# Kernel tuning notes

Measured on AMD Instinct MI355X. Metric: run time of the kernel, lower is better.

Reference implementation:

```python
import jax, jax.numpy as jnp
import numpy as np

HIDDEN = 2048
N_HEADS = 16
N_KV_HEADS = 8
HEAD_DIM = 128
MROPE_SECTION = [8, 8, 24, 24]          # sums to HEAD_DIM // 2
ROPE_THETA = 10000.0
B, S, CTX = 4, 1024, 2048
# per-frequency section index (which of the 4 position streams drives each freq)
_SEC_IDX = np.repeat(np.arange(len(MROPE_SECTION)), MROPE_SECTION)  # (HEAD_DIM//2,)


def setup_inputs() -> dict:
    key = jax.random.key(0)
    ks = jax.random.split(key, 6)
    return {
        "hidden_states": jax.random.normal(ks[0], (B, S, HIDDEN), jnp.float32),
        "Wqkv": jax.random.normal(ks[1], (HIDDEN, (N_HEADS + 2 * N_KV_HEADS) * HEAD_DIM), jnp.float32) * 0.02,
        "Wo": jax.random.normal(ks[2], (N_HEADS * HEAD_DIM, HIDDEN), jnp.float32) * 0.02,
        "ctx_k": jax.random.normal(ks[3], (B, CTX, N_KV_HEADS, HEAD_DIM), jnp.float32),
        "ctx_v": jax.random.normal(ks[4], (B, CTX, N_KV_HEADS, HEAD_DIM), jnp.float32),
        "position_ids": jax.random.randint(ks[5], (len(MROPE_SECTION), S), 0, CTX + S, jnp.int32),
    }


def _mrope_cos_sin(position_ids):
    # position_ids: (n_sections, S) int -> cos/sin of shape (S, HEAD_DIM)
    half = HEAD_DIM // 2
    inv_freq = 1.0 / (ROPE_THETA ** (jnp.arange(0, half, dtype=jnp.float32) * 2.0 / HEAD_DIM))
    freqs = position_ids.astype(jnp.float32)[:, :, None] * inv_freq[None, None, :]  # (4, S, half)
    sec = jnp.asarray(_SEC_IDX)[None, None, :]                                       # (1, 1, half)
    f = jnp.take_along_axis(freqs, jnp.broadcast_to(sec, (1,) + freqs.shape[1:]), axis=0)[0]  # (S, half)
    emb = jnp.concatenate([f, f], axis=-1)  # (S, HEAD_DIM)
    return jnp.cos(emb), jnp.sin(emb)


def _rotate_half(x):
    h = x.shape[-1] // 2
    return jnp.concatenate([-x[..., h:], x[..., :h]], axis=-1)


def reference(hidden_states, Wqkv, Wo, ctx_k, ctx_v, position_ids):
    b, s, _ = hidden_states.shape
    q_size = N_HEADS * HEAD_DIM
    kv_size = N_KV_HEADS * HEAD_DIM
    qkv = hidden_states @ Wqkv  # (B, S, q+2kv)
    q = qkv[..., :q_size].reshape(b, s, N_HEADS, HEAD_DIM)
    k = qkv[..., q_size:q_size + kv_size].reshape(b, s, N_KV_HEADS, HEAD_DIM)
    v = qkv[..., q_size + kv_size:].reshape(b, s, N_KV_HEADS, HEAD_DIM)

    cos, sin = _mrope_cos_sin(position_ids)        # (S, D) each
    cos = cos[None, :, None, :]
    sin = sin[None, :, None, :]
    q = q * cos + _rotate_half(q) * sin
    k = k * cos + _rotate_half(k) * sin

    # KV-cache concat along sequence dim
    k = jnp.concatenate([ctx_k, k], axis=1)        # (B, CTX+S, KV, D)
    v = jnp.concatenate([ctx_v, v], axis=1)

    # GQA: expand kv heads to query heads
    rep = N_HEADS // N_KV_HEADS
    k = jnp.repeat(k, rep, axis=2)                 # (B, T, H, D)
    v = jnp.repeat(v, rep, axis=2)

    scale = HEAD_DIM ** -0.5
    scores = jnp.einsum("bqhd,bkhd->bhqk", q, k) * scale  # non-causal
    probs = jax.nn.softmax(scores, axis=-1)
    out = jnp.einsum("bhqk,bkhd->bqhd", probs, v)  # (B, S, H, D)
    out = out.reshape(b, s, N_HEADS * HEAD_DIM)
    return out @ Wo
```

## Files before the change

kernel.cpp:

```cpp
#include <hip/hip_runtime.h>
#include <hip/hip_bf16.h>
#include <stdint.h>

#define NH 16
#define NKV 8
#define HD 128
#define BB 4
#define SS 1024
#define CTXL 2048
#define LT 3072
#define HID 2048
#define QKVN 4096
#define MROWS 4096

typedef __hip_bfloat16 bf16;
using f32x4 = __attribute__((ext_vector_type(4))) float;
using s16x8 = __attribute__((ext_vector_type(8))) short;

#define MFMA(a, b, c) __builtin_amdgcn_mfma_f32_16x16x32_bf16((a), (b), (c), 0, 0, 0)

__device__ __forceinline__ void gload_lds16(const void* g, void* l) {
  __builtin_amdgcn_global_load_lds((const __attribute__((address_space(1))) void*)g,
                                   (__attribute__((address_space(3))) void*)l, 16, 0, 0);
}

__device__ __forceinline__ void store_bf8(bf16* dst, const float* f) {
  bf16 tmp[8];
#pragma unroll
  for (int j = 0; j < 8; ++j) tmp[j] = __float2bfloat16(f[j]);
  __builtin_memcpy((void*)dst, (const void*)tmp, 16);
}

__device__ __forceinline__ float bf2f(short x) {
  unsigned int u = ((unsigned int)(unsigned short)x) << 16;
  float f;
  __builtin_memcpy(&f, &u, 4);
  return f;
}

#define P1_CVT 4096
#define P1_WQ (P1_CVT + 8192)
#define P1_WO (P1_WQ + 4096)
#define P1_RT (P1_WO + 256)
#define P1_CK (P1_RT + 4096)
#define P1_CV (P1_CK + 8192)

__global__ void prep1(const float* __restrict__ hs, const float* __restrict__ Wqkv,
                      const float* __restrict__ Wo, const float* __restrict__ ck,
                      const float* __restrict__ cv, const int* __restrict__ pid,
                      bf16* __restrict__ Hb, bf16* __restrict__ WqT,
                      bf16* __restrict__ WoT, bf16* __restrict__ Kf,
                      bf16* __restrict__ Vt, float* __restrict__ cosT,
                      float* __restrict__ sinT) {
  __shared__ float tile[32][33];
  const int blk = blockIdx.x, thr = threadIdx.x;
  if (blk < P1_CVT) {
    size_t tid = (size_t)blk * 256 + thr;
    const float4* p = (const float4*)(hs + tid * 8);
    float4 a = p[0], b = p[1];
    float f[8] = {a.x, a.y, a.z, a.w, b.x, b.y, b.z, b.w};
    store_bf8(Hb + tid * 8, f);
  } else if (blk < P1_WQ) {
    int j = blk - P1_CVT;
    int c0 = (j & 127) * 32, r0 = (j >> 7) * 32;
    int tx = thr & 31, ty = thr >> 5;
#pragma unroll
    for (int i = 0; i < 32; i += 8)
      tile[ty + i][tx] = Wqkv[(size_t)(r0 + ty + i) * QKVN + c0 + tx];
    __syncthreads();
#pragma unroll
    for (int i = 0; i < 32; i += 8)
      WqT[(size_t)(c0 + ty + i) * HID + r0 + tx] = __float2bfloat16(tile[tx][ty + i]);
  } else if (blk < P1_WO) {
    int j = blk - P1_WQ;
    int c0 = (j & 63) * 32, r0 = (j >> 6) * 32;
    int tx = thr & 31, ty = thr >> 5;
#pragma unroll
    for (int i = 0; i < 32; i += 8)
      tile[ty + i][tx] = Wo[(size_t)(r0 + ty + i) * 2048 + c0 + tx];
    __syncthreads();
#pragma unroll
    for (int i = 0; i < 32; i += 8)
      WoT[(size_t)(c0 + ty + i) * 2048 + r0 + tx] = __float2bfloat16(tile[tx][ty + i]);
  } else if (blk < P1_RT) {
    int tid = (blk - P1_WO) * 256 + thr;
    int j = tid & 63, s = tid >> 6;
    int sec = (j < 8) ? 0 : (j < 16) ? 1 : (j < 40) ? 2 : 3;
    float pos = (float)pid[sec * SS + s];
    float inv = __expf(-(float)j * 0.14391156831212787f);
    float a = pos * inv;
    cosT[tid] = cosf(a);
    sinT[tid] = sinf(a);
  } else if (blk < P1_CK) {
    int tid = (blk - P1_RT) * 256 + thr;
    int d8 = tid & 15, l = (tid >> 4) & 2047, h = (tid >> 15) & 7, b = tid >> 18;
    const float* s = ck + (((size_t)b * CTXL + l) * NKV + h) * HD + d8 * 8;
    const float4* p = (const float4*)s;
    float4 a = p[0], bb = p[1];
    float f[8] = {a.x, a.y, a.z, a.w, bb.x, bb.y, bb.z, bb.w};
    store_bf8(Kf + (((size_t)(b * NKV + h)) * LT + l) * HD + d8 * 8, f);
  } else {
    int j = blk - P1_CK;
    int l0 = (j & 63) * 32, d0 = ((j >> 6) & 3) * 32;
    int bz = j >> 8, b = bz >> 3, h = bz & 7;
    int tx = thr & 31, ty = thr >> 5;
#pragma unroll
    for (int i = 0; i < 32; i += 8)
      tile[ty + i][tx] =
          cv[(((size_t)b * CTXL + l0 + ty + i) * NKV + h) * HD + d0 + tx];
    __syncthreads();
#pragma unroll
    for (int i = 0; i < 32; i += 8)
      Vt[(((size_t)(b * NKV + h)) * HD + d0 + ty + i) * LT + l0 + tx] =
          __float2bfloat16(tile[tx][ty + i]);
  }
}


__global__ __launch_bounds__(512, 1) void gemm_qkv(
    const bf16* __restrict__ A, const bf16* __restrict__ BT,
    bf16* __restrict__ qkv, bf16* __restrict__ Kf, bf16* __restrict__ Vt,
    const float* __restrict__ cosT, const float* __restrict__ sinT) {
  __shared__ __attribute__((aligned(16))) char smem[132096];
  bf16* lds = (bf16*)smem;
#define lAp(s, hf) (lds + ((s)*2 + (hf)) * 8192)
#define lBp(s, hf) (lds + 32768 + ((s)*2 + (hf)) * 8192)
  const int K = HID;
  const int t = threadIdx.x;
  const int lane = t & 63, w = t >> 6;
  const int wr = w >> 2, wc = w & 3;
  const int lrow = lane & 15, kgrp = lane >> 4;
  const int lin = blockIdx.y * gridDim.x + blockIdx.x;
  const int qq = (gridDim.x * gridDim.y) >> 3;
  const int swz = (lin & 7) * qq + (lin >> 3);
  const int bx = swz % gridDim.x, by = swz / gridDim.x;
  const int m0 = by * 256, n0 = bx * 256;
  const f32x4 fz = {0.f, 0.f, 0.f, 0.f};
  f32x4 acc[8][4];
#pragma unroll
  for (int i = 0; i < 8; ++i)
#pragma unroll
    for (int j = 0; j < 4; ++j) acc[i][j] = fz;

#define STAGEH(sslot, skt, isB, shalf)                                        \
  do {                                                                        \
    _Pragma("unroll") for (int c = 0; c < 2; ++c) {                           \
      int row = w * 16 + c * 8 + (lane >> 3);                                 \
      int sch = (lane & 7) ^ (lane >> 3);                                     \
      const bf16* src =                                                       \
          (isB) ? (BT + (size_t)(n0 + (shalf)*128 + row) * K + (skt)*64 + sch * 8) \
                : (A + (size_t)(m0 + (shalf)*128 + row) * K + (skt)*64 + sch * 8); \
      bf16* dst = ((isB) ? lBp((sslot), (shalf)) : lAp((sslot), (shalf))) +   \
                  (w * 16 + c * 8) * 64;                                      \
      gload_lds16(src, dst);                                                  \
    }                                                                         \
  } while (0)

#define PHASE(cslot, qm, qn, DOST, sslot, skt, isB, shalf)                    \
  do {                                                                        \
    if (DOST) {                                                               \
      STAGEH(sslot, skt, isB, shalf);                                         \
      asm volatile("s_waitcnt vmcnt(2)" ::: "memory");                        \
    } else {                                                                  \
      asm volatile("s_waitcnt vmcnt(0)" ::: "memory");                        \
    }                                                                         \
    __builtin_amdgcn_s_barrier();                                             \
    __builtin_amdgcn_sched_barrier(0);                                        \
    s16x8 af_[4][2], bf_[2][2];                                               \
    _Pragma("unroll") for (int fi = 0; fi < 4; ++fi)                          \
        _Pragma("unroll") for (int ks = 0; ks < 2; ++ks) {                    \
      int row = (qm)*64 + fi * 16 + lrow;                                     \
      af_[fi][ks] = *(const s16x8*)&lAp(cslot, wr)[row * 64 +                 \
                                                   ((ks * 4 + kgrp) ^ (lrow & 7)) * 8]; \
    }                                                                         \
    _Pragma("unroll") for (int fj = 0; fj < 2; ++fj)                          \
        _Pragma("unroll") for (int ks = 0; ks < 2; ++ks) {                    \
      int col = (wc & 1) * 64 + (qn)*32 + fj * 16 + lrow;                     \
      bf_[fj][ks] = *(const s16x8*)&lBp(cslot, wc >> 1)[col * 64 +            \
                                                        ((ks * 4 + kgrp) ^ (lrow & 7)) * 8]; \
    }                                                                         \
    asm volatile("s_waitcnt lgkmcnt(0)" ::: "memory");                        \
    __builtin_amdgcn_sched_barrier(0);                                        \
    __builtin_amdgcn_s_setprio(1);                                            \
    _Pragma("unroll") for (int fi = 0; fi < 4; ++fi)                          \
        _Pragma("unroll") for (int fj = 0; fj < 2; ++fj)                      \
            _Pragma("unroll") for (int ks = 0; ks < 2; ++ks)                  \
                acc[(qm)*4 + fi][(qn)*2 + fj] =                               \
        MFMA(af_[fi][ks], bf_[fj][ks], acc[(qm)*4 + fi][(qn)*2 + fj]);        \
    __builtin_amdgcn_s_setprio(0);                                            \
    __builtin_amdgcn_s_barrier();                                             \
  } while (0)

  STAGEH(0, 0, 0, 0);
  STAGEH(0, 0, 1, 0);
  STAGEH(0, 0, 0, 1);
  STAGEH(0, 0, 1, 1);
  asm volatile("s_waitcnt vmcnt(0)" ::: "memory");
  __builtin_amdgcn_s_barrier();

  for (int kt = 0; kt < 32; kt += 2) {
    PHASE(0, 0, 0, true, 1, kt + 1, 0, 0);
    PHASE(0, 1, 0, true, 1, kt + 1, 1, 0);
    PHASE(0, 0, 1, true, 1, kt + 1, 0, 1);
    PHASE(0, 1, 1, true, 1, kt + 1, 1, 1);
    const bool d2 = (kt + 2 < 32);
    PHASE(1, 0, 0, d2, 0, kt + 2, 0, 0);
    PHASE(1, 1, 0, d2, 0, kt + 2, 1, 0);
    PHASE(1, 0, 1, d2, 0, kt + 2, 0, 1);
    PHASE(1, 1, 1, d2, 0, kt + 2, 1, 1);
  }
#undef PHASE
#undef STAGEH

  const int b = m0 >> 10, s0 = m0 & 1023;
  if (n0 < 2048) {
#pragma unroll
    for (int fm = 0; fm < 8; ++fm)
#pragma unroll
      for (int fn = 0; fn < 4; ++fn)
#pragma unroll
        for (int r = 0; r < 4; ++r) {
          int row = m0 + wr * 128 + fm * 16 + kgrp * 4 + r;
          int col = n0 + wc * 64 + fn * 16 + lrow;
          qkv[(size_t)row * QKVN + col] = __float2bfloat16(acc[fm][fn][r]);
        }
  } else {
    float* stage = (float*)smem;
#pragma unroll 1
    for (int hh = 0; hh < 2; ++hh) {
      __syncthreads();
      if ((wc >> 1) == hh) {
#pragma unroll
        for (int fm = 0; fm < 8; ++fm)
#pragma unroll
          for (int fn = 0; fn < 4; ++fn)
#pragma unroll
            for (int r = 0; r < 4; ++r) {
              int rr = wr * 128 + fm * 16 + kgrp * 4 + r;
              int cc = (wc & 1) * 64 + fn * 16 + lrow;
              stage[rr * 129 + cc] = acc[fm][fn][r];
            }
      }
      __syncthreads();
      if (n0 < 3072) {
        int h = ((n0 - 2048) >> 7) + hh;
#pragma unroll 4
        for (int it = 0; it < 32; ++it) {
          int idx = it * 512 + t;
          int r = idx >> 6, j = idx & 63;
          float x1 = stage[r * 129 + j], x2 = stage[r * 129 + j + 64];
          int s = s0 + r;
          float c = cosT[s * 64 + j], sn = sinT[s * 64 + j];
          bf16* dst = Kf + ((size_t)(b * NKV + h) * LT + CTXL + s) * HD;
          dst[j] = __float2bfloat16(x1 * c - x2 * sn);
          dst[j + 64] = __float2bfloat16(x2 * c + x1 * sn);
        }
      } else {
        int h = ((n0 - 3072) >> 7) + hh;
#pragma unroll 4
        for (int it = 0; it < 64; ++it) {
          int idx = it * 512 + t;
          int soff = idx & 255, d = idx >> 8;
          Vt[((size_t)(b * NKV + h) * HD + d) * LT + CTXL + s0 + soff] =
              __float2bfloat16(stage[soff * 129 + d]);
        }
      }
    }
  }
#undef lAp
#undef lBp
}

template <typename OT>
__global__ __launch_bounds__(512, 1) void gemm_bt(const bf16* __restrict__ A,
                                                  const bf16* __restrict__ BT,
                                                  OT* __restrict__ C, int M, int N,
                                                  int K) {
  __shared__ __attribute__((aligned(16))) bf16 lA[3][256][64];
  __shared__ __attribute__((aligned(16))) bf16 lB[3][128][64];
  const int t = threadIdx.x;
  const int lane = t & 63, w = t >> 6;
  const int wr = w >> 1, wc = w & 1;
  const int lrow = lane & 15, kgrp = lane >> 4;
  const int rchk = lrow & 7;
  const int lin = blockIdx.y * gridDim.x + blockIdx.x;
  const int qq = (gridDim.x * gridDim.y) >> 3;
  const int swz = (lin & 7) * qq + (lin >> 3);
  const int bx = swz % gridDim.x, by = swz / gridDim.x;
  const int m0 = by * 256, n0 = bx * 128;
  const int srow = lane >> 3;
  const int schk = (lane & 7) ^ srow;
  const f32x4 fz = {0.f, 0.f, 0.f, 0.f};
  f32x4 acc[4][4];
#pragma unroll
  for (int i = 0; i < 4; ++i)
#pragma unroll
    for (int j = 0; j < 4; ++j) acc[i][j] = fz;
  const int NTK = K >> 6;

#define GSTAGE(ib, kt)                                                      \
  do {                                                                      \
    _Pragma("unroll") for (int c = 0; c < 4; ++c) {                         \
      int ra = c * 64 + w * 8 + srow;                                       \
      gload_lds16(A + (size_t)(m0 + ra) * K + (kt)*64 + schk * 8,           \
                  &lA[ib][c * 64 + w * 8][0]);                              \
    }                                                                       \
    _Pragma("unroll") for (int c = 0; c < 2; ++c) {                         \
      int rb = c * 64 + w * 8 + srow;                                       \
      gload_lds16(BT + (size_t)(n0 + rb) * K + (kt)*64 + schk * 8,          \
                  &lB[ib][c * 64 + w * 8][0]);                              \
    }                                                                       \
  } while (0)

  GSTAGE(0, 0);
  GSTAGE(1, 1);
  int ib = 0;
  for (int kt = 0; kt < NTK; ++kt) {
    if (kt + 1 < NTK)
      asm volatile("s_waitcnt vmcnt(6) lgkmcnt(0)" ::: "memory");
    else
      asm volatile("s_waitcnt vmcnt(0) lgkmcnt(0)" ::: "memory");
    __builtin_amdgcn_s_barrier();
    __builtin_amdgcn_sched_barrier(0);
    if (kt + 2 < NTK) {
      int ib2 = ib + 2;
      if (ib2 >= 3) ib2 -= 3;
      GSTAGE(ib2, kt + 2);
    }
#pragma unroll
    for (int kk = 0; kk < 2; ++kk) {
      s16x8 af[4], bf[4];
#pragma unroll
      for (int i = 0; i < 4; ++i)
        af[i] = *(const s16x8*)&lA[ib][wr * 64 + i * 16 + lrow]
                                     [(((kk << 2) + kgrp) ^ rchk) * 8];
#pragma unroll
      for (int j = 0; j < 4; ++j)
        bf[j] = *(const s16x8*)&lB[ib][wc * 64 + j * 16 + lrow]
                                     [(((kk << 2) + kgrp) ^ rchk) * 8];
      __builtin_amdgcn_s_setprio(1);
#pragma unroll
      for (int i = 0; i < 4; ++i)
#pragma unroll
        for (int j = 0; j < 4; ++j) acc[i][j] = MFMA(af[i], bf[j], acc[i][j]);
      __builtin_amdgcn_s_setprio(0);
    }
    ++ib;
    if (ib >= 3) ib = 0;
  }
#undef GSTAGE

#pragma unroll
  for (int i = 0; i < 4; ++i)
#pragma unroll
    for (int j = 0; j < 4; ++j)
#pragma unroll
      for (int r = 0; r < 4; ++r) {
        int row = m0 + wr * 64 + i * 16 + kgrp * 4 + r;
        int col = n0 + wc * 64 + j * 16 + lrow;
        float v = acc[i][j][r];
        if constexpr (sizeof(OT) == 2)
          C[(size_t)row * N + col] = __float2bfloat16(v);
        else
          C[(size_t)row * N + col] = v;
      }
}

#define PSTR 72
#define KVB 128
#define NTT 24
#define SCALE2 0.1275174335919605f

__global__ __launch_bounds__(512, 2) void flash_attn(
    const bf16* __restrict__ qkv, const float* __restrict__ cosT,
    const float* __restrict__ sinT, const bf16* __restrict__ Kf,
    const bf16* __restrict__ Vt, bf16* __restrict__ O) {
  __shared__ __attribute__((aligned(16))) bf16 Kl[2][128][128];
  __shared__ __attribute__((aligned(16))) bf16 Vl[2][128][128];
  __shared__ __attribute__((aligned(16))) bf16 P_lds[8][16][PSTR];
  const int t = threadIdx.x, lane = t & 63, w = t >> 6;
  const int id = blockIdx.x;
  const int b = id >> 6, hk = id & 7;
  const int h = (hk << 1) | ((id >> 5) & 1);
  const int qb = (id >> 3) & 3;
  const int lrow = lane & 15, kgrp = lane >> 4;
  const bf16* Kp = Kf + (size_t)(b * NKV + hk) * LT * HD;
  const bf16* Vp = Vt + (size_t)(b * NKV + hk) * HD * LT;

  s16x8 qf[2][4];
#pragma unroll
  for (int f = 0; f < 2; ++f) {
    int srw_i = qb * 256 + w * 32 + f * 16 + lrow;
    const bf16* qrow = qkv + ((size_t)b * SS + srw_i) * QKVN + h * HD;
    s16x8 qr[4];
#pragma unroll
    for (int kd = 0; kd < 4; ++kd)
      qr[kd] = *(const s16x8*)&qrow[kd * 32 + kgrp * 8];
    const float* crow = cosT + srw_i * 64 + kgrp * 8;
    const float* srow = sinT + srw_i * 64 + kgrp * 8;
    float qv[4][8], cc[2][8], ssv[2][8];
#pragma unroll
    for (int kd = 0; kd < 4; ++kd)
#pragma unroll
      for (int j = 0; j < 8; ++j) qv[kd][j] = bf2f(qr[kd][j]);
#pragma unroll
    for (int g = 0; g < 2; ++g)
#pragma unroll
      for (int j = 0; j < 8; ++j) {
        cc[g][j] = crow[g * 32 + j];
        ssv[g][j] = srow[g * 32 + j];
      }
    bf16 o[4][8];
#pragma unroll
    for (int j = 0; j < 8; ++j) {
      o[0][j] = __float2bfloat16(qv[0][j] * cc[0][j] - qv[2][j] * ssv[0][j]);
      o[1][j] = __float2bfloat16(qv[1][j] * cc[1][j] - qv[3][j] * ssv[1][j]);
      o[2][j] = __float2bfloat16(qv[2][j] * cc[0][j] + qv[0][j] * ssv[0][j]);
      o[3][j] = __float2bfloat16(qv[3][j] * cc[1][j] + qv[1][j] * ssv[1][j]);
    }
#pragma unroll
    for (int kd = 0; kd < 4; ++kd) __builtin_memcpy(&qf[f][kd], o[kd], 16);
  }

  const f32x4 fz = {0.f, 0.f, 0.f, 0.f};
  f32x4 acc[2][8];
#pragma unroll
  for (int f = 0; f < 2; ++f)
#pragma unroll
    for (int i = 0; i < 8; ++i) acc[f][i] = fz;
  float m_[2] = {-1e30f, -1e30f}, l_[2] = {0.f, 0.f};

#define STAGE_K(buf, l0)                                                        \
  do {                                                                          \
    _Pragma("unroll") for (int c = 0; c < 4; ++c) {                             \
      int row = w * 16 + c * 4 + (lane >> 4);                                   \
      gload_lds16(Kp + (size_t)((l0) + row) * HD + ((lane & 15) ^ (row & 15)) * 8, \
                  &Kl[buf][w * 16 + c * 4][0]);                                 \
    }                                                                           \
  } while (0)
#define STAGE_V(buf, l0)                                                        \
  do {                                                                          \
    _Pragma("unroll") for (int c = 0; c < 4; ++c) {                             \
      int d = w * 16 + c * 4 + (lane >> 4);                                     \
      gload_lds16(Vp + (size_t)d * LT + (l0) + ((lane & 15) ^ (d & 15)) * 8,    \
                  &Vl[buf][w * 16 + c * 4][0]);                                 \
    }                                                                           \
  } while (0)

  STAGE_K(0, 0);
  STAGE_V(0, 0);
  __syncthreads();

  for (int tt = 0; tt < NTT; ++tt) {
    const int cur = tt & 1;
    if (tt + 1 < NTT) {
      STAGE_K(cur ^ 1, (tt + 1) * KVB);
      STAGE_V(cur ^ 1, (tt + 1) * KVB);
    }

    f32x4 sc[2][8];
#pragma unroll
    for (int f = 0; f < 2; ++f)
#pragma unroll
      for (int cf = 0; cf < 8; ++cf) sc[f][cf] = fz;
#pragma unroll
    for (int cf = 0; cf < 8; ++cf)
#pragma unroll
      for (int kd = 0; kd < 4; ++kd) {
        s16x8 kb =
            *(const s16x8*)&Kl[cur][cf * 16 + lrow][((kd * 4 + kgrp) ^ lrow) * 8];
#pragma unroll
        for (int f = 0; f < 2; ++f) sc[f][cf] = MFMA(kb, qf[f][kd], sc[f][cf]);
      }

    float mxv[2];
#pragma unroll
    for (int f = 0; f < 2; ++f) {
      float mx = sc[f][0][0];
#pragma unroll
      for (int cf = 0; cf < 8; ++cf)
#pragma unroll
        for (int r = 0; r < 4; ++r) mx = fmaxf(mx, sc[f][cf][r]);
      mx *= SCALE2;
      mx = fmaxf(mx, __shfl_xor(mx, 16, 64));
      mx = fmaxf(mx, __shfl_xor(mx, 32, 64));
      mxv[f] = mx;
    }
    bool nb = (mxv[0] > m_[0] + 8.f) || (mxv[1] > m_[1] + 8.f);
    if (__any(nb)) {
#pragma unroll
      for (int f = 0; f < 2; ++f) {
        float mn = fmaxf(m_[f], mxv[f]);
        float so = exp2f(m_[f] - mn);
        m_[f] = mn;
        l_[f] *= so;
        float sob[4];
#pragma unroll
        for (int r = 0; r < 4; ++r) sob[r] = __shfl(so, kgrp * 4 + r, 16);
#pragma unroll
        for (int nd = 0; nd < 8; ++nd)
#pragma unroll
          for (int r = 0; r < 4; ++r) acc[f][nd][r] *= sob[r];
      }
    }

    float lp[2] = {0.f, 0.f};
#pragma unroll
    for (int half = 0; half < 2; ++half) {
      s16x8 pa[2][2];
#pragma unroll
      for (int f = 0; f < 2; ++f) {
#pragma unroll
        for (int cf = 0; cf < 4; ++cf) {
          int cfs = half * 4 + cf;
          bf16 pk[4];
#pragma unroll
          for (int r = 0; r < 4; ++r) {
            float p = exp2f(sc[f][cfs][r] * SCALE2 - m_[f]);
            lp[f] += p;
            pk[r] = __float2bfloat16(p);
          }
          __builtin_memcpy((void*)&P_lds[w][lrow][cf * 16 + kgrp * 4], pk, 8);
        }
#pragma unroll
        for (int kc = 0; kc < 2; ++kc)
          pa[f][kc] = *(const s16x8*)&P_lds[w][lrow][kc * 32 + kgrp * 8];
      }
#pragma unroll
      for (int nd = 0; nd < 8; ++nd)
#pragma unroll
        for (int kc = 0; kc < 2; ++kc) {
          s16x8 vb = *(const s16x8*)&Vl[cur][nd * 16 + lrow]
                                       [((half * 8 + kc * 4 + kgrp) ^ lrow) * 8];
#pragma unroll
          for (int f = 0; f < 2; ++f) acc[f][nd] = MFMA(pa[f][kc], vb, acc[f][nd]);
        }
    }
#pragma unroll
    for (int f = 0; f < 2; ++f) l_[f] += lp[f];

    __syncthreads();
  }
#undef STAGE_K
#undef STAGE_V

  float li[2][4];
#pragma unroll
  for (int f = 0; f < 2; ++f) {
    float lv = l_[f];
    lv += __shfl_xor(lv, 16, 64);
    lv += __shfl_xor(lv, 32, 64);
#pragma unroll
    for (int r = 0; r < 4; ++r) li[f][r] = 1.f / __shfl(lv, kgrp * 4 + r, 16);
  }
#pragma unroll
  for (int f = 0; f < 2; ++f)
#pragma unroll
    for (int nd = 0; nd < 8; ++nd)
#pragma unroll
      for (int r = 0; r < 4; ++r) {
        int row = qb * 256 + w * 32 + f * 16 + kgrp * 4 + r;
        O[((size_t)b * SS + row) * 2048 + h * HD + nd * 16 + lrow] =
            __float2bfloat16(acc[f][nd][r] * li[f][r]);
      }
}


extern "C" void kernel_launch(void* const* d_in, const int* in_sizes, int n_in,
                              void* d_out, int out_size, void* d_ws, size_t ws_size,
                              hipStream_t stream) {
  const float* hs = (const float*)d_in[0];
  const float* Wqkv = (const float*)d_in[1];
  const float* Wo = (const float*)d_in[2];
  const float* ctx_k = (const float*)d_in[3];
  const float* ctx_v = (const float*)d_in[4];
  const int* pid = (const int*)d_in[5];
  float* out = (float*)d_out;
  char* ws = (char*)d_ws;

  bf16* Hb = (bf16*)(ws);
  bf16* WqT = (bf16*)(ws + 16777216);
  bf16* WoT = (bf16*)(ws + 33554432);
  bf16* qkv = (bf16*)(ws + 41943040);
  bf16* Kfull = (bf16*)(ws + 92274688);
  bf16* Vt = (bf16*)(ws + 117440512);
  float* cosT = (float*)(ws + 142606336);
  float* sinT = (float*)(ws + 142606336 + 262144);
  bf16* attn = Hb;

  prep1<<<P1_CV, 256, 0, stream>>>(hs, Wqkv, Wo, ctx_k, ctx_v, pid, Hb, WqT, WoT,
                                   Kfull, Vt, cosT, sinT);
  gemm_qkv<<<dim3(QKVN / 256, MROWS / 256), 512, 0, stream>>>(
      Hb, WqT, qkv, Kfull, Vt, cosT, sinT);
  flash_attn<<<256, 512, 0, stream>>>(qkv, cosT, sinT, Kfull, Vt, attn);
  gemm_bt<float><<<dim3(2048 / 128, MROWS / 256), 512, 0, stream>>>(
      attn, WoT, out, MROWS, 2048, HID);
}
```

Measured before the change: 292.6 us.

## Move ctx K/V and Wo conversion into QKV GEMM launch as extra blocks

The ctx_k/ctx_v bf16 conversion and the Wo transpose are moved out of the prep kernel and appended as extra blocks to the QKV GEMM launch, so this memory-bound work can run alongside the compute-bound GEMM tiles. The prep kernel shrinks and uses 512-thread blocks, each doing two transpose tiles. The GEMM grid becomes 1D with a hardcoded swizzle. A risk is that the extra blocks request the GEMM's full 132KB LDS allocation and launch-bounds occupancy of 1, which limits how many can be resident per CU.

After: 313.4 us. +7.1%, slower.

```diff
diff --git a/kernel.cpp b/kernel.cpp
--- a/kernel.cpp
+++ b/kernel.cpp
@@ -38,52 +38,36 @@
   return f;
 }
 
-#define P1_CVT 4096
-#define P1_WQ (P1_CVT + 8192)
-#define P1_WO (P1_WQ + 4096)
-#define P1_RT (P1_WO + 256)
-#define P1_CK (P1_RT + 4096)
-#define P1_CV (P1_CK + 8192)
+#define P1_CVT 2048
+#define P1_WQ (P1_CVT + 4096)
+#define P1_RT (P1_WQ + 128)
 
 __global__ void prep1(const float* __restrict__ hs, const float* __restrict__ Wqkv,
-                      const float* __restrict__ Wo, const float* __restrict__ ck,
-                      const float* __restrict__ cv, const int* __restrict__ pid,
-                      bf16* __restrict__ Hb, bf16* __restrict__ WqT,
-                      bf16* __restrict__ WoT, bf16* __restrict__ Kf,
-                      bf16* __restrict__ Vt, float* __restrict__ cosT,
+                      const int* __restrict__ pid, bf16* __restrict__ Hb,
+                      bf16* __restrict__ WqT, float* __restrict__ cosT,
                       float* __restrict__ sinT) {
-  __shared__ float tile[32][33];
-  const int blk = blockIdx.x, thr = threadIdx.x;
+  __shared__ float tile[2][32][33];
+  const int blk = blockIdx.x, t = threadIdx.x;
   if (blk < P1_CVT) {
-    size_t tid = (size_t)blk * 256 + thr;
+    size_t tid = (size_t)blk * 512 + t;
     const float4* p = (const float4*)(hs + tid * 8);
     float4 a = p[0], b = p[1];
     float f[8] = {a.x, a.y, a.z, a.w, b.x, b.y, b.z, b.w};
     store_bf8(Hb + tid * 8, f);
   } else if (blk < P1_WQ) {
-    int j = blk - P1_CVT;
-    int c0 = (j & 127) * 32, r0 = (j >> 7) * 32;
-    int tx = thr & 31, ty = thr >> 5;
+    int j2 = (blk - P1_CVT) * 2 + (t >> 8);
+    int c0 = (j2 & 127) * 32, r0 = (j2 >> 7) * 32;
+    int tt = t & 255, tx = tt & 31, ty = tt >> 5, sl = t >> 8;
 #pragma unroll
     for (int i = 0; i < 32; i += 8)
-      tile[ty + i][tx] = Wqkv[(size_t)(r0 + ty + i) * QKVN + c0 + tx];
+      tile[sl][ty + i][tx] = Wqkv[(size_t)(r0 + ty + i) * QKVN + c0 + tx];
     __syncthreads();
 #pragma unroll
     for (int i = 0; i < 32; i += 8)
-      WqT[(size_t)(c0 + ty + i) * HID + r0 + tx] = __float2bfloat16(tile[tx][ty + i]);
-  } else if (blk < P1_WO) {
-    int j = blk - P1_WQ;
-    int c0 = (j & 63) * 32, r0 = (j >> 6) * 32;
-    int tx = thr & 31, ty = thr >> 5;
-#pragma unroll
-    for (int i = 0; i < 32; i += 8)
-      tile[ty + i][tx] = Wo[(size_t)(r0 + ty + i) * 2048 + c0 + tx];
-    __syncthreads();
-#pragma unroll
-    for (int i = 0; i < 32; i += 8)
-      WoT[(size_t)(c0 + ty + i) * 2048 + r0 + tx] = __float2bfloat16(tile[tx][ty + i]);
-  } else if (blk < P1_RT) {
-    int tid = (blk - P1_WO) * 256 + thr;
+      WqT[(size_t)(c0 + ty + i) * HID + r0 + tx] =
+          __float2bfloat16(tile[sl][tx][ty + i]);
+  } else {
+    int tid = (blk - P1_WQ) * 512 + t;
     int j = tid & 63, s = tid >> 6;
     int sec = (j < 8) ? 0 : (j < 16) ? 1 : (j < 40) ? 2 : 3;
     float pos = (float)pid[sec * SS + s];
@@ -91,49 +75,75 @@
     float a = pos * inv;
     cosT[tid] = cosf(a);
     sinT[tid] = sinf(a);
-  } else if (blk < P1_CK) {
-    int tid = (blk - P1_RT) * 256 + thr;
-    int d8 = tid & 15, l = (tid >> 4) & 2047, h = (tid >> 15) & 7, b = tid >> 18;
-    const float* s = ck + (((size_t)b * CTXL + l) * NKV + h) * HD + d8 * 8;
-    const float4* p = (const float4*)s;
-    float4 a = p[0], bb = p[1];
-    float f[8] = {a.x, a.y, a.z, a.w, bb.x, bb.y, bb.z, bb.w};
-    store_bf8(Kf + (((size_t)(b * NKV + h)) * LT + l) * HD + d8 * 8, f);
-  } else {
-    int j = blk - P1_CK;
-    int l0 = (j & 63) * 32, d0 = ((j >> 6) & 3) * 32;
-    int bz = j >> 8, b = bz >> 3, h = bz & 7;
-    int tx = thr & 31, ty = thr >> 5;
-#pragma unroll
-    for (int i = 0; i < 32; i += 8)
-      tile[ty + i][tx] =
-          cv[(((size_t)b * CTXL + l0 + ty + i) * NKV + h) * HD + d0 + tx];
-    __syncthreads();
-#pragma unroll
-    for (int i = 0; i < 32; i += 8)
-      Vt[(((size_t)(b * NKV + h)) * HD + d0 + ty + i) * LT + l0 + tx] =
-          __float2bfloat16(tile[tx][ty + i]);
-  }
-}
-
+  }
+}
+
+#define GQ_CK 256
+#define GQ_CV 2304
+#define GQ_WO 6400
+#define GQ_TOT 8448
 
 __global__ __launch_bounds__(512, 1) void gemm_qkv(
     const bf16* __restrict__ A, const bf16* __restrict__ BT,
     bf16* __restrict__ qkv, bf16* __restrict__ Kf, bf16* __restrict__ Vt,
-    const float* __restrict__ cosT, const float* __restrict__ sinT) {
+    const float* __restrict__ cosT, const float* __restrict__ sinT,
+    const float* __restrict__ Wo, bf16* __restrict__ WoT,
+    const float* __restrict__ ck, const float* __restrict__ cv) {
   __shared__ __attribute__((aligned(16))) char smem[132096];
+  const int id = blockIdx.x;
+  const int t = threadIdx.x;
+
+  if (id >= GQ_CK) {
+    if (id < GQ_CV) {
+      int tid = (id - GQ_CK) * 512 + t;
+      int d8 = tid & 15, l = (tid >> 4) & 2047, h = (tid >> 15) & 7, b = tid >> 18;
+      const float* s = ck + (((size_t)b * CTXL + l) * NKV + h) * HD + d8 * 8;
+      const float4* p = (const float4*)s;
+      float4 a = p[0], bb = p[1];
+      float f[8] = {a.x, a.y, a.z, a.w, bb.x, bb.y, bb.z, bb.w};
+      store_bf8(Kf + (((size_t)(b * NKV + h)) * LT + l) * HD + d8 * 8, f);
+    } else if (id < GQ_WO) {
+      float(*tile)[32][33] = (float(*)[32][33])smem;
+      int j2 = (id - GQ_CV) * 2 + (t >> 8);
+      int l0 = (j2 & 63) * 32, d0 = ((j2 >> 6) & 3) * 32;
+      int bz = j2 >> 8, b = bz >> 3, h = bz & 7;
+      int tt = t & 255, tx = tt & 31, ty = tt >> 5, sl = t >> 8;
+#pragma unroll
+      for (int i = 0; i < 32; i += 8)
+        tile[sl][ty + i][tx] =
+            cv[(((size_t)b * CTXL + l0 + ty + i) * NKV + h) * HD + d0 + tx];
+      __syncthreads();
+#pragma unroll
+      for (int i = 0; i < 32; i += 8)
+        Vt[(((size_t)(b * NKV + h)) * HD + d0 + ty + i) * LT + l0 + tx] =
+            __float2bfloat16(tile[sl][tx][ty + i]);
+    } else {
+      float(*tile)[32][33] = (float(*)[32][33])smem;
+      int j2 = (id - GQ_WO) * 2 + (t >> 8);
+      int c0 = (j2 & 63) * 32, r0 = (j2 >> 6) * 32;
+      int tt = t & 255, tx = tt & 31, ty = tt >> 5, sl = t >> 8;
+#pragma unroll
+      for (int i = 0; i < 32; i += 8)
+        tile[sl][ty + i][tx] = Wo[(size_t)(r0 + ty + i) * 2048 + c0 + tx];
+      __syncthreads();
+#pragma unroll
+      for (int i = 0; i < 32; i += 8)
+        WoT[(size_t)(c0 + ty + i) * 2048 + r0 + tx] =
+            __float2bfloat16(tile[sl][tx][ty + i]);
+    }
+    return;
+  }
+
   bf16* lds = (bf16*)smem;
 #define lAp(s, hf) (lds + ((s)*2 + (hf)) * 8192)
 #define lBp(s, hf) (lds + 32768 + ((s)*2 + (hf)) * 8192)
   const int K = HID;
-  const int t = threadIdx.x;
   const int lane = t & 63, w = t >> 6;
   const int wr = w >> 2, wc = w & 3;
   const int lrow = lane & 15, kgrp = lane >> 4;
-  const int lin = blockIdx.y * gridDim.x + blockIdx.x;
-  const int qq = (gridDim.x * gridDim.y) >> 3;
-  const int swz = (lin & 7) * qq + (lin >> 3);
-  const int bx = swz % gridDim.x, by = swz / gridDim.x;
+  const int lin = id;
+  const int swz = (lin & 7) * 32 + (lin >> 3);
+  const int bx = swz & 15, by = swz >> 4;
   const int m0 = by * 256, n0 = bx * 256;
   const f32x4 fz = {0.f, 0.f, 0.f, 0.f};
   f32x4 acc[8][4];
@@ -588,10 +598,9 @@
   float* sinT = (float*)(ws + 142606336 + 262144);
   bf16* attn = Hb;
 
-  prep1<<<P1_CV, 256, 0, stream>>>(hs, Wqkv, Wo, ctx_k, ctx_v, pid, Hb, WqT, WoT,
-                                   Kfull, Vt, cosT, sinT);
-  gemm_qkv<<<dim3(QKVN / 256, MROWS / 256), 512, 0, stream>>>(
-      Hb, WqT, qkv, Kfull, Vt, cosT, sinT);
+  prep1<<<P1_RT, 512, 0, stream>>>(hs, Wqkv, pid, Hb, WqT, cosT, sinT);
+  gemm_qkv<<<GQ_TOT, 512, 0, stream>>>(Hb, WqT, qkv, Kfull, Vt, cosT, sinT, Wo,
+                                       WoT, ctx_k, ctx_v);
   flash_attn<<<256, 512, 0, stream>>>(qkv, cosT, sinT, Kfull, Vt, attn);
   gemm_bt<float><<<dim3(2048 / 128, MROWS / 256), 512, 0, stream>>>(
       attn, WoT, out, MROWS, 2048, HID);
```

## Restructure output projection GEMM into phased double-buffered schedule with 2x4 warp grid

Applied to the files above, without the earlier changes.

Replaces the generic triple-buffered output-projection GEMM with a specialized kernel that uses two LDS buffers and splits each K-tile into four quarter phases. Global-to-LDS loads for the next tile are issued piecewise across those phases, each with its own vmcnt wait and barrier. The warp layout changes from 4x2 to 2x4, so each warp now computes 128x32 instead of 64x64. The aim is to interleave loads with MFMA work more finely and cut LDS footprint, at the cost of many more barriers per tile and a less square per-warp fragment shape.

After: 303.6 us. 3.8% more time.

```diff
diff --git a/kernel.cpp b/kernel.cpp
--- a/kernel.cpp
+++ b/kernel.cpp
@@ -116,7 +116,6 @@
   }
 }
 
-
 __global__ __launch_bounds__(512, 1) void gemm_qkv(
     const bf16* __restrict__ A, const bf16* __restrict__ BT,
     bf16* __restrict__ qkv, bf16* __restrict__ Kf, bf16* __restrict__ Vt,
@@ -271,98 +270,110 @@
 #undef lBp
 }
 
-template <typename OT>
-__global__ __launch_bounds__(512, 1) void gemm_bt(const bf16* __restrict__ A,
+__global__ __launch_bounds__(512, 1) void gemm_op(const bf16* __restrict__ A,
                                                   const bf16* __restrict__ BT,
-                                                  OT* __restrict__ C, int M, int N,
-                                                  int K) {
-  __shared__ __attribute__((aligned(16))) bf16 lA[3][256][64];
-  __shared__ __attribute__((aligned(16))) bf16 lB[3][128][64];
+                                                  float* __restrict__ C) {
+  __shared__ __attribute__((aligned(16))) bf16 lA[2][256][64];
+  __shared__ __attribute__((aligned(16))) bf16 lB[2][128][64];
+  const int K = HID, N = 2048;
   const int t = threadIdx.x;
   const int lane = t & 63, w = t >> 6;
-  const int wr = w >> 1, wc = w & 1;
+  const int wr = w >> 2, wc = w & 3;
   const int lrow = lane & 15, kgrp = lane >> 4;
-  const int rchk = lrow & 7;
   const int lin = blockIdx.y * gridDim.x + blockIdx.x;
   const int qq = (gridDim.x * gridDim.y) >> 3;
   const int swz = (lin & 7) * qq + (lin >> 3);
   const int bx = swz % gridDim.x, by = swz / gridDim.x;
   const int m0 = by * 256, n0 = bx * 128;
-  const int srow = lane >> 3;
-  const int schk = (lane & 7) ^ srow;
   const f32x4 fz = {0.f, 0.f, 0.f, 0.f};
-  f32x4 acc[4][4];
-#pragma unroll
-  for (int i = 0; i < 4; ++i)
-#pragma unroll
-    for (int j = 0; j < 4; ++j) acc[i][j] = fz;
-  const int NTK = K >> 6;
-
-#define GSTAGE(ib, kt)                                                      \
-  do {                                                                      \
-    _Pragma("unroll") for (int c = 0; c < 4; ++c) {                         \
-      int ra = c * 64 + w * 8 + srow;                                       \
-      gload_lds16(A + (size_t)(m0 + ra) * K + (kt)*64 + schk * 8,           \
-                  &lA[ib][c * 64 + w * 8][0]);                              \
-    }                                                                       \
-    _Pragma("unroll") for (int c = 0; c < 2; ++c) {                         \
-      int rb = c * 64 + w * 8 + srow;                                       \
-      gload_lds16(BT + (size_t)(n0 + rb) * K + (kt)*64 + schk * 8,          \
-                  &lB[ib][c * 64 + w * 8][0]);                              \
-    }                                                                       \
+  f32x4 acc[8][2];
+#pragma unroll
+  for (int i = 0; i < 8; ++i)
+#pragma unroll
+    for (int j = 0; j < 2; ++j) acc[i][j] = fz;
+
+#define OSA(sslot, skt, half)                                                 \
+  do {                                                                        \
+    _Pragma("unroll") for (int c = 0; c < 2; ++c) {                           \
+      int row = w * 16 + c * 8 + (lane >> 3);                                 \
+      int sch = (lane & 7) ^ (lane >> 3);                                     \
+      gload_lds16(A + (size_t)(m0 + (half)*128 + row) * K + (skt)*64 + sch * 8, \
+                  &lA[sslot][(half)*128 + w * 16 + c * 8][0]);                \
+    }                                                                         \
   } while (0)
-
-  GSTAGE(0, 0);
-  GSTAGE(1, 1);
-  int ib = 0;
-  for (int kt = 0; kt < NTK; ++kt) {
-    if (kt + 1 < NTK)
-      asm volatile("s_waitcnt vmcnt(6) lgkmcnt(0)" ::: "memory");
-    else
-      asm volatile("s_waitcnt vmcnt(0) lgkmcnt(0)" ::: "memory");
-    __builtin_amdgcn_s_barrier();
-    __builtin_amdgcn_sched_barrier(0);
-    if (kt + 2 < NTK) {
-      int ib2 = ib + 2;
-      if (ib2 >= 3) ib2 -= 3;
-      GSTAGE(ib2, kt + 2);
-    }
-#pragma unroll
-    for (int kk = 0; kk < 2; ++kk) {
-      s16x8 af[4], bf[4];
-#pragma unroll
-      for (int i = 0; i < 4; ++i)
-        af[i] = *(const s16x8*)&lA[ib][wr * 64 + i * 16 + lrow]
-                                     [(((kk << 2) + kgrp) ^ rchk) * 8];
-#pragma unroll
-      for (int j = 0; j < 4; ++j)
-        bf[j] = *(const s16x8*)&lB[ib][wc * 64 + j * 16 + lrow]
-                                     [(((kk << 2) + kgrp) ^ rchk) * 8];
-      __builtin_amdgcn_s_setprio(1);
-#pragma unroll
-      for (int i = 0; i < 4; ++i)
-#pragma unroll
-        for (int j = 0; j < 4; ++j) acc[i][j] = MFMA(af[i], bf[j], acc[i][j]);
-      __builtin_amdgcn_s_setprio(0);
-    }
-    ++ib;
-    if (ib >= 3) ib = 0;
+#define OSB(sslot, skt)                                                       \
+  do {                                                                        \
+    _Pragma("unroll") for (int c = 0; c < 2; ++c) {                           \
+      int row = w * 16 + c * 8 + (lane >> 3);                                 \
+      int sch = (lane & 7) ^ (lane >> 3);                                     \
+      gload_lds16(BT + (size_t)(n0 + row) * K + (skt)*64 + sch * 8,           \
+                  &lB[sslot][w * 16 + c * 8][0]);                             \
+    }                                                                         \
+  } while (0)
+
+#define OPHASE(cslot, qm, qn, DOST, STG, VMC)                                 \
+  do {                                                                        \
+    if (DOST) {                                                               \
+      STG;                                                                    \
+      asm volatile("s_waitcnt vmcnt(" #VMC ")" ::: "memory");                 \
+    } else {                                                                  \
+      asm volatile("s_waitcnt vmcnt(0)" ::: "memory");                        \
+    }                                                                         \
+    __builtin_amdgcn_s_barrier();                                             \
+    __builtin_amdgcn_sched_barrier(0);                                        \
+    s16x8 af_[4][2], bf_[2];                                                  \
+    _Pragma("unroll") for (int fi = 0; fi < 4; ++fi)                          \
+        _Pragma("unroll") for (int ks = 0; ks < 2; ++ks) {                    \
+      int row = wr * 128 + (qm)*64 + fi * 16 + lrow;                          \
+      af_[fi][ks] = *(const s16x8*)&lA[cslot][row]                            \
+                                       [((ks * 4 + kgrp) ^ (lrow & 7)) * 8];  \
+    }                                                                         \
+    _Pragma("unroll") for (int ks = 0; ks < 2; ++ks) {                        \
+      int col = wc * 32 + (qn)*16 + lrow;                                     \
+      bf_[ks] = *(const s16x8*)&lB[cslot][col]                                \
+                                   [((ks * 4 + kgrp) ^ (lrow & 7)) * 8];      \
+    }                                                                         \
+    asm volatile("s_waitcnt lgkmcnt(0)" ::: "memory");                        \
+    __builtin_amdgcn_sched_barrier(0);                                        \
+    __builtin_amdgcn_s_setprio(1);                                            \
+    _Pragma("unroll") for (int fi = 0; fi < 4; ++fi)                          \
+        _Pragma("unroll") for (int ks = 0; ks < 2; ++ks)                      \
+            acc[(qm)*4 + fi][qn] =                                            \
+        MFMA(af_[fi][ks], bf_[ks], acc[(qm)*4 + fi][qn]);                     \
+    __builtin_amdgcn_s_setprio(0);                                            \
+    __builtin_amdgcn_s_barrier();                                             \
+  } while (0)
+
+  OSA(0, 0, 0);
+  OSA(0, 0, 1);
+  OSB(0, 0);
+  asm volatile("s_waitcnt vmcnt(0)" ::: "memory");
+  __builtin_amdgcn_s_barrier();
+
+  for (int kt = 0; kt < 32; kt += 2) {
+    OPHASE(0, 0, 0, true, OSA(1, kt + 1, 0), 2);
+    OPHASE(0, 1, 0, true, OSA(1, kt + 1, 1), 4);
+    OPHASE(0, 0, 1, true, OSB(1, kt + 1), 6);
+    OPHASE(0, 1, 1, false, (void)0, 6);
+    const bool d2 = (kt + 2 < 32);
+    OPHASE(1, 0, 0, d2, OSA(0, kt + 2, 0), 2);
+    OPHASE(1, 1, 0, d2, OSA(0, kt + 2, 1), 4);
+    OPHASE(1, 0, 1, d2, OSB(0, kt + 2), 6);
+    OPHASE(1, 1, 1, false, (void)0, 6);
   }
-#undef GSTAGE
-
-#pragma unroll
-  for (int i = 0; i < 4; ++i)
-#pragma unroll
-    for (int j = 0; j < 4; ++j)
+#undef OPHASE
+#undef OSA
+#undef OSB
+
+#pragma unroll
+  for (int fm = 0; fm < 8; ++fm)
+#pragma unroll
+    for (int fn = 0; fn < 2; ++fn)
 #pragma unroll
       for (int r = 0; r < 4; ++r) {
-        int row = m0 + wr * 64 + i * 16 + kgrp * 4 + r;
-        int col = n0 + wc * 64 + j * 16 + lrow;
-        float v = acc[i][j][r];
-        if constexpr (sizeof(OT) == 2)
-          C[(size_t)row * N + col] = __float2bfloat16(v);
-        else
-          C[(size_t)row * N + col] = v;
+        int row = m0 + wr * 128 + fm * 16 + kgrp * 4 + r;
+        int col = n0 + wc * 32 + fn * 16 + lrow;
+        C[(size_t)row * N + col] = acc[fm][fn][r];
       }
 }
 
@@ -593,6 +604,5 @@
   gemm_qkv<<<dim3(QKVN / 256, MROWS / 256), 512, 0, stream>>>(
       Hb, WqT, qkv, Kfull, Vt, cosT, sinT);
   flash_attn<<<256, 512, 0, stream>>>(qkv, cosT, sinT, Kfull, Vt, attn);
-  gemm_bt<float><<<dim3(2048 / 128, MROWS / 256), 512, 0, stream>>>(
-      attn, WoT, out, MROWS, 2048, HID);
-}
+  gemm_op<<<dim3(2048 / 128, MROWS / 256), 512, 0, stream>>>(attn, WoT, out);
+}
```
